# Optimization experiments

Measured on AMD Instinct MI355X. Metric: run time of the kernel, lower is better.

The kernel has to match this reference:

```python
import jax, jax.numpy as jnp
import numpy as np

B, C, N = 8, 64, 4096

def setup_inputs() -> dict:
    key = jax.random.key(0)
    k1, k2, k3 = jax.random.split(key, 3)
    k = jax.random.normal(k1, (B, C, N), dtype=jnp.float32)
    q = jax.random.normal(k2, (B, C, N), dtype=jnp.float32)
    v = jax.random.normal(k3, (B, C, N), dtype=jnpp.float32) if False else jax.random.normal(k3, (B, C, N), dtype=jnp.float32)
    return {"k": k, "q": q, "v": v}

def reference(k, q, v):
    input_dim = k.shape[1]  # C
    # similarity = k^T @ q : [B, N, N]
    scores = jnp.einsum('bcn,bcm->bnm', k, q) / jnp.sqrt(jnp.float32(input_dim))
    attn = jax.nn.softmax(scores, axis=-1)  # softmax over last dim (query positions m)
    # out = attn @ v^T : [B, N, C], then transpose back to [B, C, N]
    out = jnp.einsum('bnm,bcm->bcn', attn, v)
    return out
```

## Files before the change

### kernel.cpp

```cpp
#include <hip/hip_runtime.h>
#include <stdint.h>

typedef __attribute__((ext_vector_type(8)))  __bf16        bf16x8;
typedef __attribute__((ext_vector_type(8)))  unsigned short u16x8;
typedef __attribute__((ext_vector_type(4)))  float          f32x4;
typedef __attribute__((ext_vector_type(16))) float          f32x16;
typedef __attribute__((ext_vector_type(4)))  unsigned int   u32x4;

#define NB 8
#define NC 64
#define NN 4096
#define NCHUNK 64
#define CHUNK_U16 4096
#define SPLITQ 4

#define EXP2F(x) __builtin_amdgcn_exp2f(x)

__device__ __forceinline__ unsigned short f2bf(float x) {
    unsigned int u = __builtin_bit_cast(unsigned int, x);
    u += 0x7fffu + ((u >> 16) & 1u);
    return (unsigned short)(u >> 16);
}
__device__ __forceinline__ unsigned int pk2(float a, float b) {
    unsigned short x = __builtin_bit_cast(unsigned short, (__bf16)a);
    unsigned short y = __builtin_bit_cast(unsigned short, (__bf16)b);
    return (unsigned int)x | ((unsigned int)y << 16);
}

__global__ __launch_bounds__(256) void prepass(
    const float* __restrict__ qp, const float* __restrict__ vp,
    unsigned short* __restrict__ qfo, unsigned short* __restrict__ vfo)
{
    __shared__ float lt[64][68];
    const int orig = blockIdx.x;
    const int bid = (orig & 7) * 64 + (orig >> 3);
    const int b = bid >> 6, mc = bid & 63;
    const int m0 = mc * 64;
    const int tid = threadIdx.x;
    const float* qb = qp + (size_t)b * NC * NN;
    const float* vb = vp + (size_t)b * NC * NN;
    unsigned short* qfc = qfo + (size_t)bid * CHUNK_U16;
    unsigned short* vfc = vfo + (size_t)bid * CHUNK_U16;

    #pragma unroll
    for (int rep = 0; rep < 4; ++rep) {
        int idx = tid + 256 * rep;
        int c = idx >> 4, m4 = (idx & 15) << 2;
        f32x4 xv = *reinterpret_cast<const f32x4*>(qb + (size_t)c * NN + m0 + m4);
        lt[m4+0][c] = xv[0]; lt[m4+1][c] = xv[1];
        lt[m4+2][c] = xv[2]; lt[m4+3][c] = xv[3];
    }
    __syncthreads();
    #pragma unroll
    for (int rep = 0; rep < 2; ++rep) {
        int fid = tid + 256 * rep;
        int l = fid & 63, kk = (fid >> 6) & 3, mt = fid >> 8;
        int m = 32 * mt + (l & 31), c0 = 16 * kk + 8 * (l >> 5);
        u16x8 ov;
        #pragma unroll
        for (int e = 0; e < 8; ++e) ov[e] = f2bf(lt[m][c0 + e]);
        *reinterpret_cast<u16x8*>(qfc + (size_t)fid * 8) = ov;
    }
    __syncthreads();
    #pragma unroll
    for (int rep = 0; rep < 4; ++rep) {
        int idx = tid + 256 * rep;
        int c = idx >> 4, m4 = (idx & 15) << 2;
        f32x4 xv = *reinterpret_cast<const f32x4*>(vb + (size_t)c * NN + m0 + m4);
        *reinterpret_cast<f32x4*>(&lt[c][m4]) = xv;
    }
    __syncthreads();
    #pragma unroll
    for (int rep = 0; rep < 2; ++rep) {
        int fid = tid + 256 * rep;
        int l = fid & 63, kt = (fid >> 6) & 3, ct = fid >> 8;
        int c = 32 * ct + (l & 31), mm = 16 * kt + 8 * (l >> 5);
        u16x8 ov;
        #pragma unroll
        for (int e = 0; e < 8; ++e) ov[e] = f2bf(lt[c][mm + e]);
        *reinterpret_cast<u16x8*>(vfc + (size_t)fid * 8) = ov;
    }
}

template<int SPLITQ_T>
__global__ __launch_bounds__(256, 3) void attn7(
    const float* __restrict__ kp,
    const unsigned short* __restrict__ qfo,
    const unsigned short* __restrict__ vfo,
    float* __restrict__ part, float* __restrict__ lp)
{
    constexpr int CPQ_T = NCHUNK / SPLITQ_T;
    constexpr int TG = NN / 128;
    constexpr int PER_XCD = SPLITQ_T * TG;
    __shared__ unsigned short sb[2][2 * CHUNK_U16];

    const int orig = blockIdx.x;
    const int bid  = (orig & 7) * PER_XCD + (orig >> 3);
    const int b    = bid / PER_XCD;
    const int rest = bid % PER_XCD;
    const int qid  = rest / TG;
    const int tg   = rest % TG;
    const int bn0  = tg * 128;
    const int tid = threadIdx.x;
    const int w = tid >> 6, l = tid & 63;
    const int lo5 = l & 31, hi = l >> 5;
    const int nrow = bn0 + 32 * w + lo5;

    const float kscale = 0.125f * 1.44269504088896f;
    const float* kb = kp + (size_t)b * NC * NN;
    bf16x8 kf[4];
    #pragma unroll
    for (int kk = 0; kk < 4; ++kk) {
        u16x8 t;
        #pragma unroll
        for (int e = 0; e < 8; ++e)
            t[e] = __builtin_bit_cast(unsigned short,
                      (__bf16)(kscale * kb[(size_t)(16 * kk + 8 * hi + e) * NN + nrow]));
        kf[kk] = __builtin_bit_cast(bf16x8, t);
    }

    const unsigned short* qg = qfo + (size_t)(b * NCHUNK + qid * CPQ_T) * CHUNK_U16;
    const unsigned short* vg = vfo + (size_t)(b * NCHUNK + qid * CPQ_T) * CHUNK_U16;

    auto stage = [&](int mcr, int buf) {
        const unsigned short* gq = qg + (size_t)mcr * CHUNK_U16;
        const unsigned short* gv = vg + (size_t)mcr * CHUNK_U16;
        #pragma unroll
        for (int j = 0; j < 2; ++j) {
            int off = w * 1024 + j * 512 + l * 8;
            __builtin_amdgcn_global_load_lds(
                (const __attribute__((address_space(1))) void*)(gq + off),
                (__attribute__((address_space(3))) void*)(&sb[buf][w * 1024 + j * 512]),
                16, 0, 0);
            __builtin_amdgcn_global_load_lds(
                (const __attribute__((address_space(1))) void*)(gv + off),
                (__attribute__((address_space(3))) void*)(&sb[buf][CHUNK_U16 + w * 1024 + j * 512]),
                16, 0, 0);
        }
    };

    stage(0, 0);
    __syncthreads();

    f32x16 zro;
    #pragma unroll
    for (int r = 0; r < 16; ++r) zro[r] = 0.f;
    f32x16 o0 = zro, o1 = zro;
    float sum = 0.f;

    for (int mcr = 0; mcr < CPQ_T; ++mcr) {
        const int cur = mcr & 1;
        if (mcr + 1 < CPQ_T) stage(mcr + 1, cur ^ 1);
        const unsigned short* qb_ = &sb[cur][0];
        const unsigned short* vb_ = &sb[cur][CHUNK_U16];

        u16x8 a[8];
        #pragma unroll
        for (int f = 0; f < 8; ++f)
            a[f] = *reinterpret_cast<const u16x8*>(qb_ + (f * 64 + l) * 8);

        f32x16 s0 = __builtin_amdgcn_mfma_f32_32x32x16_bf16(__builtin_bit_cast(bf16x8, a[0]), kf[0], zro, 0, 0, 0);
        f32x16 s1 = __builtin_amdgcn_mfma_f32_32x32x16_bf16(__builtin_bit_cast(bf16x8, a[4]), kf[0], zro, 0, 0, 0);
        #pragma unroll
        for (int kk = 1; kk < 4; ++kk) {
            s0 = __builtin_amdgcn_mfma_f32_32x32x16_bf16(__builtin_bit_cast(bf16x8, a[kk]),     kf[kk], s0, 0, 0, 0);
            s1 = __builtin_amdgcn_mfma_f32_32x32x16_bf16(__builtin_bit_cast(bf16x8, a[4 + kk]), kf[kk], s1, 0, 0, 0);
        }

        #pragma unroll
        for (int f = 0; f < 8; ++f)
            a[f] = *reinterpret_cast<const u16x8*>(vb_ + (f * 64 + l) * 8);

        #pragma unroll
        for (int r = 0; r < 16; ++r) { s0[r] = EXP2F(s0[r]); sum += s0[r]; }
        #pragma unroll
        for (int r = 0; r < 16; ++r) { s1[r] = EXP2F(s1[r]); sum += s1[r]; }

        #pragma unroll
        for (int kt = 0; kt < 4; ++kt) {
            const f32x16& sm = (kt < 2) ? s0 : s1;
            const int qA = 2 * (kt & 1);
            unsigned int wA0 = pk2(sm[4*qA+0], sm[4*qA+1]);
            unsigned int wA1 = pk2(sm[4*qA+2], sm[4*qA+3]);
            unsigned int wB0 = pk2(sm[4*qA+4], sm[4*qA+5]);
            unsigned int wB1 = pk2(sm[4*qA+6], sm[4*qA+7]);
            unsigned int e0 = (unsigned int)__shfl_xor((int)(hi ? wA0 : wB0), 32);
            unsigned int e1 = (unsigned int)__shfl_xor((int)(hi ? wA1 : wB1), 32);
            u32x4 pf = hi ? (u32x4){e0, e1, wB0, wB1} : (u32x4){wA0, wA1, e0, e1};
            bf16x8 pB = __builtin_bit_cast(bf16x8, pf);
            o0 = __builtin_amdgcn_mfma_f32_32x32x16_bf16(__builtin_bit_cast(bf16x8, a[kt]),     pB, o0, 0, 0, 0);
            o1 = __builtin_amdgcn_mfma_f32_32x32x16_bf16(__builtin_bit_cast(bf16x8, a[4 + kt]), pB, o1, 0, 0, 0);
        }
        __syncthreads();
    }

    sum += (float)__shfl_xor(sum, 32);
    const int t64 = (bn0 >> 6) + (w >> 1);
    const int rowoff = 32 * (w & 1);
    const int pidx = (b * 64 + t64) * SPLITQ_T + qid;
    float* po = part + (size_t)pidx * 4096;
    #pragma unroll
    for (int r = 0; r < 16; ++r) {
        int cb = (r & 3) + 8 * (r >> 2) + 4 * hi;
        po[cb * 64 + rowoff + lo5]        = o0[r];
        po[(32 + cb) * 64 + rowoff + lo5] = o1[r];
    }
    if (hi == 0) lp[(size_t)pidx * 64 + rowoff + lo5] = sum;
}

__global__ __launch_bounds__(256) void combine2(
    const float* __restrict__ part, const float* __restrict__ lp,
    float* __restrict__ outp, int splitq)
{
    __shared__ float sinv[64];
    const int orig = blockIdx.x;
    const int bid = (orig & 7) * 64 + (orig >> 3);
    const int b = bid >> 6, tile = bid & 63;
    const int n0 = tile * 64;
    const int t = threadIdx.x;
    const int pb = bid * splitq;

    if (t < 64) {
        float L = 0.f;
        for (int q = 0; q < splitq; ++q) L += lp[(size_t)(pb + q) * 64 + t];
        sinv[t] = 1.0f / L;
    }
    __syncthreads();

    float* ob = outp + (size_t)b * NC * NN;
    #pragma unroll
    for (int it = 0; it < 4; ++it) {
        int idx = it * 1024 + t * 4;
        int ch = idx >> 6, r0 = idx & 63;
        f32x4 acc = (f32x4){0.f, 0.f, 0.f, 0.f};
        for (int q = 0; q < splitq; ++q) {
            f32x4 v = *reinterpret_cast<const f32x4*>(part + (size_t)(pb + q) * 4096 + idx);
            acc += v;
        }
        f32x4 res;
        #pragma unroll
        for (int u = 0; u < 4; ++u) res[u] = acc[u] * sinv[r0 + u];
        *reinterpret_cast<f32x4*>(ob + (size_t)ch * NN + n0 + r0) = res;
    }
}

__global__ __launch_bounds__(128) void attn2(
    const float* __restrict__ kp,
    const unsigned short* __restrict__ qfo,
    const unsigned short* __restrict__ vfo,
    float* __restrict__ outp)
{
    __shared__ unsigned short sb[2][2 * CHUNK_U16];
    const int orig = blockIdx.x;
    const int bid  = (orig & 7) * 64 + (orig >> 3);
    const int b = bid >> 6, nt = bid & 63;
    const int n0 = nt * 64;
    const int tid = threadIdx.x;
    const int w = tid >> 6, l = tid & 63;
    const int lo5 = l & 31, hi = l >> 5;
    const int nrow = n0 + 32 * w + lo5;
    const float kscale = 0.125f * 1.44269504088896f;
    const float* kb = kp + (size_t)b * NC * NN;
    bf16x8 kf[4];
    #pragma unroll
    for (int kk = 0; kk < 4; ++kk) {
        u16x8 t;
        #pragma unroll
        for (int e = 0; e < 8; ++e)
            t[e] = f2bf(kscale * kb[(size_t)(16 * kk + 8 * hi + e) * NN + nrow]);
        kf[kk] = __builtin_bit_cast(bf16x8, t);
    }
    const unsigned short* qg = qfo + (size_t)(b * 64) * CHUNK_U16;
    const unsigned short* vg = vfo + (size_t)(b * 64) * CHUNK_U16;
    auto stage = [&](int mc, int buf) {
        const unsigned short* gq = qg + (size_t)mc * CHUNK_U16;
        const unsigned short* gv = vg + (size_t)mc * CHUNK_U16;
        #pragma unroll
        for (int i = 0; i < 4; ++i) {
            int seg = w * 4 + i;
            int off = seg * 512 + l * 8;
            __builtin_amdgcn_global_load_lds(
                (const __attribute__((address_space(1))) void*)(gq + off),
                (__attribute__((address_space(3))) void*)(&sb[buf][seg * 512]), 16, 0, 0);
            __builtin_amdgcn_global_load_lds(
                (const __attribute__((address_space(1))) void*)(gv + off),
                (__attribute__((address_space(3))) void*)(&sb[buf][CHUNK_U16 + seg * 512]), 16, 0, 0);
        }
    };
    stage(0, 0);
    __syncthreads();
    f32x16 o0, o1;
    #pragma unroll
    for (int r = 0; r < 16; ++r) { o0[r] = 0.f; o1[r] = 0.f; }
    float m_run = -1e30f, l_run = 0.f;
    for (int mc = 0; mc < NCHUNK; ++mc) {
        const int cur = mc & 1;
        if (mc + 1 < NCHUNK) stage(mc + 1, cur ^ 1);
        const unsigned short* qb_ = &sb[cur][0];
        const unsigned short* vb_ = &sb[cur][CHUNK_U16];
        f32x16 s0, s1;
        #pragma unroll
        for (int r = 0; r < 16; ++r) { s0[r] = 0.f; s1[r] = 0.f; }
        #pragma unroll
        for (int kk = 0; kk < 4; ++kk) {
            u16x8 a0 = *reinterpret_cast<const u16x8*>(qb_ + ((0 * 4 + kk) * 64 + l) * 8);
            u16x8 a1 = *reinterpret_cast<const u16x8*>(qb_ + ((1 * 4 + kk) * 64 + l) * 8);
            s0 = __builtin_amdgcn_mfma_f32_32x32x16_bf16(__builtin_bit_cast(bf16x8, a0), kf[kk], s0, 0, 0, 0);
            s1 = __builtin_amdgcn_mfma_f32_32x32x16_bf16(__builtin_bit_cast(bf16x8, a1), kf[kk], s1, 0, 0, 0);
        }
        float pmax = s0[0];
        #pragma unroll
        for (int r = 1; r < 16; ++r) pmax = fmaxf(pmax, s0[r]);
        #pragma unroll
        for (int r = 0; r < 16; ++r) pmax = fmaxf(pmax, s1[r]);
        pmax = fmaxf(pmax, (float)__shfl_xor(pmax, 32));
        const float mn = fmaxf(m_run, pmax);
        const float alpha = EXP2F(m_run - mn);
        float sum = 0.f;
        #pragma unroll
        for (int r = 0; r < 16; ++r) { s0[r] = EXP2F(s0[r] - mn); sum += s0[r]; }
        #pragma unroll
        for (int r = 0; r < 16; ++r) { s1[r] = EXP2F(s1[r] - mn); sum += s1[r]; }
        sum += (float)__shfl_xor(sum, 32);
        l_run = l_run * alpha + sum;
        m_run = mn;
        #pragma unroll
        for (int r = 0; r < 16; ++r) { o0[r] *= alpha; o1[r] *= alpha; }
        #pragma unroll
        for (int kt = 0; kt < 4; ++kt) {
            const f32x16& sm = (kt < 2) ? s0 : s1;
            const int qA = 2 * (kt & 1);
            unsigned int dA0 = pk2(sm[4 * qA + 0], sm[4 * qA + 1]);
            unsigned int dA1 = pk2(sm[4 * qA + 2], sm[4 * qA + 3]);
            unsigned int dB0 = pk2(sm[4 * qA + 4], sm[4 * qA + 5]);
            unsigned int dB1 = pk2(sm[4 * qA + 6], sm[4 * qA + 7]);
            unsigned int sA0 = (unsigned int)__shfl_xor((int)dA0, 32);
            unsigned int sA1 = (unsigned int)__shfl_xor((int)dA1, 32);
            unsigned int sB0 = (unsigned int)__shfl_xor((int)dB0, 32);
            unsigned int sB1 = (unsigned int)__shfl_xor((int)dB1, 32);
            u32x4 pf;
            if (hi == 0) pf = (u32x4){dA0, dA1, sA0, sA1};
            else         pf = (u32x4){sB0, sB1, dB0, dB1};
            bf16x8 pB = __builtin_bit_cast(bf16x8, pf);
            u16x8 v0 = *reinterpret_cast<const u16x8*>(vb_ + ((0 * 4 + kt) * 64 + l) * 8);
            u16x8 v1 = *reinterpret_cast<const u16x8*>(vb_ + ((1 * 4 + kt) * 64 + l) * 8);
            o0 = __builtin_amdgcn_mfma_f32_32x32x16_bf16(__builtin_bit_cast(bf16x8, v0), pB, o0, 0, 0, 0);
            o1 = __builtin_amdgcn_mfma_f32_32x32x16_bf16(__builtin_bit_cast(bf16x8, v1), pB, o1, 0, 0, 0);
        }
        __syncthreads();
    }
    const float inv = 1.0f / l_run;
    float* ob = outp + (size_t)b * NC * NN;
    #pragma unroll
    for (int r = 0; r < 16; ++r) {
        int cb = (r & 3) + 8 * (r >> 2) + 4 * hi;
        ob[(size_t)cb * NN + n0 + 32 * w + lo5]        = o0[r] * inv;
        ob[(size_t)(32 + cb) * NN + n0 + 32 * w + lo5] = o1[r] * inv;
    }
}

__global__ __launch_bounds__(256) void attn_fwd(
    const float* __restrict__ kp, const float* __restrict__ qp,
    const float* __restrict__ vp, float* __restrict__ outp)
{
    __shared__ unsigned short qs[8][64][8];
    __shared__ unsigned short vs[8][64][8];
    __shared__ unsigned short ps[4][2][64][8];
    const int orig = blockIdx.x;
    const int bid  = (orig & 7) * 64 + (orig >> 3);
    const int b  = bid >> 6;
    const int n0 = (bid & 63) * 64;
    const int tid = threadIdx.x;
    const int w = tid >> 6, l = tid & 63, g = l >> 4, j = l & 15;
    const float* kb = kp + (size_t)b * NC * NN;
    const float* qb = qp + (size_t)b * NC * NN;
    const float* vb = vp + (size_t)b * NC * NN;
    bf16x8 ak[2];
    #pragma unroll
    for (int kk = 0; kk < 2; ++kk) {
        u16x8 tmp;
        #pragma unroll
        for (int e = 0; e < 8; ++e)
            tmp[e] = f2bf(kb[(size_t)(32*kk + 8*g + e) * NN + (n0 + 16*w + j)]);
        ak[kk] = __builtin_bit_cast(bf16x8, tmp);
    }
    f32x4 o[4];
    float m_run[4], l_run[4];
    #pragma unroll
    for (int ct = 0; ct < 4; ++ct) o[ct] = (f32x4){0.f,0.f,0.f,0.f};
    #pragma unroll
    for (int r = 0; r < 4; ++r) { m_run[r] = -1e30f; l_run[r] = 0.0f; }
    for (int m0 = 0; m0 < NN; m0 += 64) {
        __syncthreads();
        #pragma unroll
        for (int it = 0; it < 4; ++it) {
            int f = tid + 256*it;
            int c = f >> 4, m4 = (f & 15) << 2;
            f32x4 qv = *reinterpret_cast<const f32x4*>(qb + (size_t)c*NN + m0 + m4);
            f32x4 vv = *reinterpret_cast<const f32x4*>(vb + (size_t)c*NN + m0 + m4);
            int kkq = c >> 5, eq = c & 7, gq = (c >> 3) & 3, tq = m4 >> 4;
            #pragma unroll
            for (int u = 0; u < 4; ++u)
                qs[kkq*4 + tq][16*gq + ((m4 + u) & 15)][eq] = f2bf(qv[u]);
            int ctv = c >> 4, jv = c & 15, kkv = m4 >> 5, gv = (m4 >> 3) & 3, ev = m4 & 7;
            #pragma unroll
            for (int u = 0; u < 4; ++u)
                vs[kkv*4 + ctv][16*gv + jv][ev + u] = f2bf(vv[u]);
        }
        __syncthreads();
        f32x4 s[4];
        #pragma unroll
        for (int t = 0; t < 4; ++t) {
            f32x4 acc = (f32x4){0.f,0.f,0.f,0.f};
            #pragma unroll
            for (int kk = 0; kk < 2; ++kk) {
                u16x8 raw = *reinterpret_cast<const u16x8*>(&qs[kk*4 + t][l][0]);
                acc = __builtin_amdgcn_mfma_f32_16x16x32_bf16(ak[kk], __builtin_bit_cast(bf16x8, raw), acc, 0,0,0);
            }
            s[t] = acc * 0.125f;
        }
        float alpha[4];
        #pragma unroll
        for (int r = 0; r < 4; ++r) {
            float m1 = fmaxf(fmaxf(s[0][r], s[1][r]), fmaxf(s[2][r], s[3][r]));
            #pragma unroll
            for (int off = 1; off < 16; off <<= 1) m1 = fmaxf(m1, __shfl_xor(m1, off));
            float mn = fmaxf(m_run[r], m1);
            alpha[r] = __expf(m_run[r] - mn);
            m_run[r] = mn;
            float acc = 0.0f;
            #pragma unroll
            for (int t = 0; t < 4; ++t) { float p = __expf(s[t][r] - mn); s[t][r] = p; acc += p; }
            #pragma unroll
            for (int off = 1; off < 16; off <<= 1) acc += __shfl_xor(acc, off);
            l_run[r] = l_run[r] * alpha[r] + acc;
        }
        {
            int srcl = (j >> 2) << 4;
            float a0 = __shfl(alpha[0], srcl), a1 = __shfl(alpha[1], srcl);
            float a2 = __shfl(alpha[2], srcl), a3 = __shfl(alpha[3], srcl);
            int rs = j & 3;
            float ac = (rs==0)?a0:(rs==1)?a1:(rs==2)?a2:a3;
            #pragma unroll
            for (int ct = 0; ct < 4; ++ct) o[ct] *= ac;
        }
        #pragma unroll
        for (int t = 0; t < 4; ++t) {
            int m = 16*t + j;
            #pragma unroll
            for (int r = 0; r < 4; ++r)
                ps[w][m >> 5][((m >> 3) & 3)*16 + 4*g + r][m & 7] = f2bf(s[t][r]);
        }
        asm volatile("s_waitcnt lgkmcnt(0)" ::: "memory");
        #pragma unroll
        for (int kk2 = 0; kk2 < 2; ++kk2) {
            u16x8 rp = *reinterpret_cast<const u16x8*>(&ps[w][kk2][l][0]);
            bf16x8 bp = __builtin_bit_cast(bf16x8, rp);
            #pragma unroll
            for (int ct = 0; ct < 4; ++ct) {
                u16x8 rv = *reinterpret_cast<const u16x8*>(&vs[kk2*4 + ct][l][0]);
                o[ct] = __builtin_amdgcn_mfma_f32_16x16x32_bf16(__builtin_bit_cast(bf16x8, rv), bp, o[ct], 0,0,0);
            }
        }
    }
    {
        int srcl = (j >> 2) << 4;
        float l0 = __shfl(l_run[0], srcl), l1 = __shfl(l_run[1], srcl);
        float l2 = __shfl(l_run[2], srcl), l3 = __shfl(l_run[3], srcl);
        int rs = j & 3;
        float lc = (rs==0)?l0:(rs==1)?l1:(rs==2)?l2:l3;
        float inv = 1.0f / lc;
        #pragma unroll
        for (int ct = 0; ct < 4; ++ct)
            #pragma unroll
            for (int r = 0; r < 4; ++r)
                outp[(size_t)b*NC*NN + (size_t)(16*ct + 4*g + r)*NN + (n0 + 16*w + j)] = o[ct][r] * inv;
    }
}

extern "C" void kernel_launch(void* const* d_in, const int* in_sizes, int n_in,
                              void* d_out, int out_size, void* d_ws, size_t ws_size,
                              hipStream_t stream) {
    const float* kp = (const float*)d_in[0];
    const float* qp = (const float*)d_in[1];
    const float* vp = (const float*)d_in[2];
    float* op = (float*)d_out;
    const size_t FRAG_BYTES = (size_t)2 * NB * NCHUNK * CHUNK_U16 * sizeof(unsigned short);
    unsigned short* qfo = (unsigned short*)d_ws;
    unsigned short* vfo = qfo + (size_t)NB * NCHUNK * CHUNK_U16;

    const size_t NEED = FRAG_BYTES
        + (size_t)NB * 64 * SPLITQ * 4096 * sizeof(float)
        + (size_t)NB * 64 * SPLITQ * 64 * sizeof(float);

    if (ws_size >= NEED) {
        float* part = (float*)((char*)d_ws + FRAG_BYTES);
        float* lpp  = part + (size_t)NB * 64 * SPLITQ * 4096;
        hipLaunchKernelGGL(prepass, dim3(NB * NCHUNK), dim3(256), 0, stream, qp, vp, qfo, vfo);
        hipLaunchKernelGGL(attn7<SPLITQ>, dim3(NB * SPLITQ * (NN / 128)), dim3(256), 0, stream,
                           kp, qfo, vfo, part, lpp);
        hipLaunchKernelGGL(combine2, dim3(NB * 64), dim3(256), 0, stream, part, lpp, op, SPLITQ);
    } else if (ws_size >= FRAG_BYTES) {
        hipLaunchKernelGGL(prepass, dim3(NB * NCHUNK), dim3(256), 0, stream, qp, vp, qfo, vfo);
        hipLaunchKernelGGL(attn2, dim3(NB * NCHUNK), dim3(128), 0, stream, kp, qfo, vfo, op);
    } else {
        hipLaunchKernelGGL(attn_fwd, dim3(512), dim3(256), 0, stream, kp, qp, vp, op);
    }
}
```

Before: 68.87 us.

## Load V fragments directly from global, swap lane halves with permlane32

```diff
diff --git a/kernel.cpp b/kernel.cpp
--- a/kernel.cpp
+++ b/kernel.cpp
@@ -83,7 +83,7 @@
 }
 
 template<int SPLITQ_T>
-__global__ __launch_bounds__(256, 3) void attn7(
+__global__ __launch_bounds__(256, 3) void attn8(
     const float* __restrict__ kp,
     const unsigned short* __restrict__ qfo,
     const unsigned short* __restrict__ vfo,
@@ -92,7 +92,7 @@
     constexpr int CPQ_T = NCHUNK / SPLITQ_T;
     constexpr int TG = NN / 128;
     constexpr int PER_XCD = SPLITQ_T * TG;
-    __shared__ unsigned short sb[2][2 * CHUNK_U16];
+    __shared__ unsigned short sq[2][CHUNK_U16];
 
     const int orig = blockIdx.x;
     const int bid  = (orig & 7) * PER_XCD + (orig >> 3);
@@ -122,24 +122,19 @@
     const unsigned short* qg = qfo + (size_t)(b * NCHUNK + qid * CPQ_T) * CHUNK_U16;
     const unsigned short* vg = vfo + (size_t)(b * NCHUNK + qid * CPQ_T) * CHUNK_U16;
 
-    auto stage = [&](int mcr, int buf) {
+    auto stage_q = [&](int mcr, int buf) {
         const unsigned short* gq = qg + (size_t)mcr * CHUNK_U16;
-        const unsigned short* gv = vg + (size_t)mcr * CHUNK_U16;
         #pragma unroll
         for (int j = 0; j < 2; ++j) {
             int off = w * 1024 + j * 512 + l * 8;
             __builtin_amdgcn_global_load_lds(
                 (const __attribute__((address_space(1))) void*)(gq + off),
-                (__attribute__((address_space(3))) void*)(&sb[buf][w * 1024 + j * 512]),
+                (__attribute__((address_space(3))) void*)(&sq[buf][w * 1024 + j * 512]),
                 16, 0, 0);
-            __builtin_amdgcn_global_load_lds(
-                (const __attribute__((address_space(1))) void*)(gv + off),
-                (__attribute__((address_space(3))) void*)(&sb[buf][CHUNK_U16 + w * 1024 + j * 512]),
-                16, 0, 0);
         }
     };
 
-    stage(0, 0);
+    stage_q(0, 0);
     __syncthreads();
 
     f32x16 zro;
@@ -150,14 +145,19 @@
 
     for (int mcr = 0; mcr < CPQ_T; ++mcr) {
         const int cur = mcr & 1;
-        if (mcr + 1 < CPQ_T) stage(mcr + 1, cur ^ 1);
-        const unsigned short* qb_ = &sb[cur][0];
-        const unsigned short* vb_ = &sb[cur][CHUNK_U16];
+        if (mcr + 1 < CPQ_T) stage_q(mcr + 1, cur ^ 1);
+        const unsigned short* qb_ = &sq[cur][0];
+        const unsigned short* vc  = vg + (size_t)mcr * CHUNK_U16;
 
         u16x8 a[8];
         #pragma unroll
         for (int f = 0; f < 8; ++f)
             a[f] = *reinterpret_cast<const u16x8*>(qb_ + (f * 64 + l) * 8);
+
+        u16x8 vf[8];
+        #pragma unroll
+        for (int f = 0; f < 8; ++f)
+            vf[f] = *reinterpret_cast<const u16x8*>(vc + (f * 64 + l) * 8);
 
         f32x16 s0 = __builtin_amdgcn_mfma_f32_32x32x16_bf16(__builtin_bit_cast(bf16x8, a[0]), kf[0], zro, 0, 0, 0);
         f32x16 s1 = __builtin_amdgcn_mfma_f32_32x32x16_bf16(__builtin_bit_cast(bf16x8, a[4]), kf[0], zro, 0, 0, 0);
@@ -167,29 +167,37 @@
             s1 = __builtin_amdgcn_mfma_f32_32x32x16_bf16(__builtin_bit_cast(bf16x8, a[4 + kk]), kf[kk], s1, 0, 0, 0);
         }
 
-        #pragma unroll
-        for (int f = 0; f < 8; ++f)
-            a[f] = *reinterpret_cast<const u16x8*>(vb_ + (f * 64 + l) * 8);
-
-        #pragma unroll
-        for (int r = 0; r < 16; ++r) { s0[r] = EXP2F(s0[r]); sum += s0[r]; }
-        #pragma unroll
-        for (int r = 0; r < 16; ++r) { s1[r] = EXP2F(s1[r]); sum += s1[r]; }
+        float ps0 = 0.f, ps1 = 0.f, ps2 = 0.f, ps3 = 0.f;
+        #pragma unroll
+        for (int r = 0; r < 16; r += 4) {
+            s0[r]   = EXP2F(s0[r]);   ps0 += s0[r];
+            s0[r+1] = EXP2F(s0[r+1]); ps1 += s0[r+1];
+            s0[r+2] = EXP2F(s0[r+2]); ps2 += s0[r+2];
+            s0[r+3] = EXP2F(s0[r+3]); ps3 += s0[r+3];
+        }
+        #pragma unroll
+        for (int r = 0; r < 16; r += 4) {
+            s1[r]   = EXP2F(s1[r]);   ps0 += s1[r];
+            s1[r+1] = EXP2F(s1[r+1]); ps1 += s1[r+1];
+            s1[r+2] = EXP2F(s1[r+2]); ps2 += s1[r+2];
+            s1[r+3] = EXP2F(s1[r+3]); ps3 += s1[r+3];
+        }
+        sum += (ps0 + ps1) + (ps2 + ps3);
 
         #pragma unroll
         for (int kt = 0; kt < 4; ++kt) {
             const f32x16& sm = (kt < 2) ? s0 : s1;
             const int qA = 2 * (kt & 1);
-            unsigned int wA0 = pk2(sm[4*qA+0], sm[4*qA+1]);
-            unsigned int wA1 = pk2(sm[4*qA+2], sm[4*qA+3]);
-            unsigned int wB0 = pk2(sm[4*qA+4], sm[4*qA+5]);
-            unsigned int wB1 = pk2(sm[4*qA+6], sm[4*qA+7]);
-            unsigned int e0 = (unsigned int)__shfl_xor((int)(hi ? wA0 : wB0), 32);
-            unsigned int e1 = (unsigned int)__shfl_xor((int)(hi ? wA1 : wB1), 32);
-            u32x4 pf = hi ? (u32x4){e0, e1, wB0, wB1} : (u32x4){wA0, wA1, e0, e1};
+            unsigned int w0 = pk2(sm[4*qA+0], sm[4*qA+1]);
+            unsigned int w1 = pk2(sm[4*qA+2], sm[4*qA+3]);
+            unsigned int w2 = pk2(sm[4*qA+4], sm[4*qA+5]);
+            unsigned int w3 = pk2(sm[4*qA+6], sm[4*qA+7]);
+            asm volatile("v_permlane32_swap_b32 %0, %1" : "+v"(w0), "+v"(w2));
+            asm volatile("v_permlane32_swap_b32 %0, %1" : "+v"(w1), "+v"(w3));
+            u32x4 pf = (u32x4){w0, w1, w2, w3};
             bf16x8 pB = __builtin_bit_cast(bf16x8, pf);
-            o0 = __builtin_amdgcn_mfma_f32_32x32x16_bf16(__builtin_bit_cast(bf16x8, a[kt]),     pB, o0, 0, 0, 0);
-            o1 = __builtin_amdgcn_mfma_f32_32x32x16_bf16(__builtin_bit_cast(bf16x8, a[4 + kt]), pB, o1, 0, 0, 0);
+            o0 = __builtin_amdgcn_mfma_f32_32x32x16_bf16(__builtin_bit_cast(bf16x8, vf[kt]),     pB, o0, 0, 0, 0);
+            o1 = __builtin_amdgcn_mfma_f32_32x32x16_bf16(__builtin_bit_cast(bf16x8, vf[4 + kt]), pB, o1, 0, 0, 0);
         }
         __syncthreads();
     }
@@ -497,7 +505,7 @@
         float* part = (float*)((char*)d_ws + FRAG_BYTES);
         float* lpp  = part + (size_t)NB * 64 * SPLITQ * 4096;
         hipLaunchKernelGGL(prepass, dim3(NB * NCHUNK), dim3(256), 0, stream, qp, vp, qfo, vfo);
-        hipLaunchKernelGGL(attn7<SPLITQ>, dim3(NB * SPLITQ * (NN / 128)), dim3(256), 0, stream,
+        hipLaunchKernelGGL(attn8<SPLITQ>, dim3(NB * SPLITQ * (NN / 128)), dim3(256), 0, stream,
                            kp, qfo, vfo, part, lpp);
         hipLaunchKernelGGL(combine2, dim3(NB * 64), dim3(256), 0, stream, part, lpp, op, SPLITQ);
     } else if (ws_size >= FRAG_BYTES) {
```

After: 65.73 us, median of 2. 4.6% less time.
